# Kernel tuning notes

Hardware: AMD Instinct MI355X
Metric: run time of the kernel (lower is better)

Reference implementation:

```python
import jax, jax.numpy as jnp
import numpy as np

HEADS = 8
DIM_HEAD = 64
NB_FEATURES = 256
CHUNK = 128          # chunk size used by performer's causal_linear_attention_noncuda
EPS_KERNEL = 1e-4    # eps in softmax_kernel feature map
EPS_DENOM = 1e-6     # eps added to k_cumsum in the denominator


def softmax_kernel(data, proj, is_query):
    # FAVOR+ positive softmax random features (performer_pytorch.softmax_kernel)
    # data: [B,H,N,D], proj: [M,D]
    d = data.shape[-1]
    normalizer = d ** -0.25
    ratio = proj.shape[0] ** -0.5
    data_dash = jnp.einsum('bhnd,md->bhnm', data * normalizer, proj)
    # ||x||^2 / (2*sqrt(d))
    diag = jnp.sum(data * data, axis=-1, keepdims=True) * 0.5 * (normalizer ** 2)
    if is_query:
        m = jax.lax.stop_gradient(jnp.max(data_dash, axis=-1, keepdims=True))
    else:
        m = jax.lax.stop_gradient(jnp.max(data_dash, axis=(-1, -2), keepdims=True))
    return ratio * (jnp.exp(data_dash - diag - m) + EPS_KERNEL)


def causal_linear_attention(qp, kp, v, chunk=CHUNK):
    # Chunked causal linear attention (O(N) in seq len):
    # out_i = q'_i . S_i / (q'_i . z_i), S_i = sum_{j<=i} k'_j v_j^T, z_i = cumsum k'_j
    B, H, N, M = qp.shape
    E = v.shape[-1]
    C = N // chunk

    def to_chunks(x):
        return x.reshape(B, H, C, chunk, x.shape[-1]).transpose(2, 0, 1, 3, 4)

    qc, kc, vc = to_chunks(qp), to_chunks(kp), to_chunks(v)
    k0 = jnp.zeros((B, H, M), qp.dtype)
    s0 = jnp.zeros((B, H, M, E), qp.dtype)

    def step(carry, inp):
        k_last, s_last = carry
        q, k, vv = inp  # [B,H,c,M], [B,H,c,M], [B,H,c,E]
        k_cum = k_last[:, :, None, :] + jnp.cumsum(k, axis=2)           # [B,H,c,M]
        d_inv = 1.0 / jnp.einsum('bhnm,bhnm->bhn', q, k_cum + EPS_DENOM)
        ctx = jnp.einsum('bhnm,bhne->bhnme', k, vv)                      # [B,H,c,M,E]
        s_cum = s_last[:, :, None] + jnp.cumsum(ctx, axis=2)             # [B,H,c,M,E]
        out = jnp.einsum('bhnme,bhnm,bhn->bhne', s_cum, q, d_inv)        # [B,H,c,E]
        return (k_cum[:, :, -1, :], s_cum[:, :, -1]), out

    _, outs = jax.lax.scan(step, (k0, s0), (qc, kc, vc))  # [C,B,H,c,E]
    return outs.transpose(1, 2, 0, 3, 4).reshape(B, H, N, E)


def setup_inputs() -> dict:
    key = jax.random.key(0)
    k1, k2, k3, k4 = jax.random.split(key, 4)
    B, N, D = 4, 2048, 512
    return {
        'query': jax.random.normal(k1, (B, N, D), jnp.float32),
        'key': jax.random.normal(k2, (B, N, D), jnp.float32),
        'value': jax.random.normal(k3, (B, N, D), jnp.float32),
        'projection': jax.random.normal(k4, (NB_FEATURES, DIM_HEAD), jnp.float32),
    }


def reference(query, key, value, projection):
    B, N, D = query.shape

    def split(x):  # [B,N,D] -> [B,H,N,Dh]
        return x.reshape(B, N, HEADS, DIM_HEAD).transpose(0, 2, 1, 3)

    q, k, v = split(query), split(key), split(value)
    qp = softmax_kernel(q, projection, is_query=True)
    kp = softmax_kernel(k, projection, is_query=False)
    out = causal_linear_attention(qp, kp, v)
    return out.transpose(0, 2, 1, 3).reshape(B, N, D)
```

## Files before the change

### kernel.cpp

```cpp
#include <hip/hip_runtime.h>
#include <math.h>

#define BB 4
#define NN 2048
#define DD 512
#define HH 8
#define DH 64
#define MM 256
#define BH 32
#define CHK 128
#define NCH 16
#define ROWS (BH*NN)

constexpr float NRM   = 0.35355339059327373f;
constexpr float RATIO = 0.0625f;
constexpr float EPSK  = 1e-4f;
constexpr float EPSD  = 1e-6f;

#define OFFB_QP   ((size_t)0)
#define OFFB_SP   ((size_t)33554432)
#define OFFB_KP   (OFFB_SP + (size_t)16777216)
#define OFFB_VT   (OFFB_KP + (size_t)33554432)
#define OFFB_Z    (OFFB_VT + (size_t)8388608)
#define OFFB_KMP  (OFFB_Z  + (size_t)524288)

typedef __attribute__((ext_vector_type(8))) short short8;
typedef __attribute__((ext_vector_type(4))) float f32x4;

__device__ __forceinline__ float b2f(ushort u) {
  union { float f; unsigned int i; } x; x.i = ((unsigned int)u) << 16; return x.f;
}
__device__ __forceinline__ ushort f2b(float f) {
  unsigned int u = __float_as_uint(f);
  unsigned int r = (u + 0x7FFFu + ((u >> 16) & 1u)) >> 16;
  return (ushort)r;
}

#define MFMA(a,b,c) __builtin_amdgcn_mfma_f32_16x16x32_bf16(a, b, c, 0, 0, 0)

template<int MODE>
__device__ __forceinline__ void featm_body(const float* __restrict__ inp,
                                           const float* __restrict__ proj,
                                           char* __restrict__ ws,
                                           char* lds, int blk) {
  ushort* xh = (ushort*)lds;
  ushort* xl = xh + 64*72;
  ushort* ps = xl + 64*72;
  ushort* qt = ps;
  float* diag_s = (float*)(lds + 55296);
  float (*wmax)[4] = (float(*)[4])(lds + 55552);
  float* kred = (float*)(lds + 56576);

  const int t  = threadIdx.x;
  const int w  = t >> 6;
  const int l  = t & 63;
  const int lq = l >> 4;
  const int ln = l & 15;

  const int rowbase = blk * 64;
  const int bh = rowbase >> 11;
  const int b  = bh >> 3, h = bh & 7;
  const int n0 = rowbase & (NN - 1);

  {
    const int r  = t >> 2;
    const int c0 = (t & 3) * 16;
    const float* src = inp + ((size_t)(b*NN + n0 + r))*DD + h*DH + c0;
    float vv[16];
    #pragma unroll
    for (int j = 0; j < 4; ++j) {
      float4 v = *(const float4*)(src + j*4);
      vv[4*j+0] = v.x*NRM; vv[4*j+1] = v.y*NRM;
      vv[4*j+2] = v.z*NRM; vv[4*j+3] = v.w*NRM;
    }
    float s = 0.f;
    ushort hi[16], lo[16];
    #pragma unroll
    for (int j = 0; j < 16; ++j) {
      s += vv[j]*vv[j];
      hi[j] = f2b(vv[j]);
      lo[j] = f2b(vv[j] - b2f(hi[j]));
    }
    *(short8*)(xh + r*72 + c0)     = *(short8*)&hi[0];
    *(short8*)(xh + r*72 + c0 + 8) = *(short8*)&hi[8];
    *(short8*)(xl + r*72 + c0)     = *(short8*)&lo[0];
    *(short8*)(xl + r*72 + c0 + 8) = *(short8*)&lo[8];
    s += __shfl_xor(s, 1); s += __shfl_xor(s, 2);
    if ((t & 3) == 0) diag_s[r] = 0.5f * s;
  }
  #pragma unroll
  for (int ld = 0; ld < 4; ++ld) {
    int flat = t + 256*ld;
    int r = flat >> 2, c0 = (flat & 3) * 16;
    const float* src = proj + (size_t)r*DH + c0;
    ushort hv[16];
    #pragma unroll
    for (int j = 0; j < 4; ++j) {
      float4 v = *(const float4*)(src + j*4);
      hv[4*j+0] = f2b(v.x); hv[4*j+1] = f2b(v.y);
      hv[4*j+2] = f2b(v.z); hv[4*j+3] = f2b(v.w);
    }
    *(short8*)(ps + r*72 + c0)     = *(short8*)&hv[0];
    *(short8*)(ps + r*72 + c0 + 8) = *(short8*)&hv[8];
  }
  __syncthreads();

  f32x4 acc[4][4];
  #pragma unroll
  for (int mt = 0; mt < 4; ++mt)
    #pragma unroll
    for (int nt = 0; nt < 4; ++nt) acc[mt][nt] = (f32x4){0.f,0.f,0.f,0.f};

  #pragma unroll
  for (int kk = 0; kk < 2; ++kk) {
    short8 ah[4], al[4];
    #pragma unroll
    for (int mt = 0; mt < 4; ++mt) {
      ah[mt] = *(const short8*)(xh + (mt*16 + ln)*72 + kk*32 + lq*8);
      al[mt] = *(const short8*)(xl + (mt*16 + ln)*72 + kk*32 + lq*8);
    }
    #pragma unroll
    for (int nt = 0; nt < 4; ++nt) {
      short8 bf = *(const short8*)(ps + (w*64 + nt*16 + ln)*72 + kk*32 + lq*8);
      #pragma unroll
      for (int mt = 0; mt < 4; ++mt) {
        acc[mt][nt] = MFMA(al[mt], bf, acc[mt][nt]);
        acc[mt][nt] = MFMA(ah[mt], bf, acc[mt][nt]);
      }
    }
  }

  if (MODE == 1) {
    float mx = -1e30f;
    #pragma unroll
    for (int mt = 0; mt < 4; ++mt)
      #pragma unroll
      for (int nt = 0; nt < 4; ++nt)
        #pragma unroll
        for (int reg = 0; reg < 4; ++reg) mx = fmaxf(mx, acc[mt][nt][reg]);
    #pragma unroll
    for (int m = 1; m < 64; m <<= 1) mx = fmaxf(mx, __shfl_xor(mx, m));
    if (l == 0) kred[w] = mx;
    __syncthreads();
    if (t == 0)
      ((float*)(ws + OFFB_KMP))[blk] =
        fmaxf(fmaxf(kred[0], kred[1]), fmaxf(kred[2], kred[3]));
    return;
  }

  if (MODE == 0) {
    #pragma unroll
    for (int mt = 0; mt < 4; ++mt)
      #pragma unroll
      for (int reg = 0; reg < 4; ++reg) {
        float m = acc[mt][0][reg];
        #pragma unroll
        for (int nt = 1; nt < 4; ++nt) m = fmaxf(m, acc[mt][nt][reg]);
        m = fmaxf(m, __shfl_xor(m, 1));
        m = fmaxf(m, __shfl_xor(m, 2));
        m = fmaxf(m, __shfl_xor(m, 4));
        m = fmaxf(m, __shfl_xor(m, 8));
        if (ln == 0) wmax[mt*16 + lq*4 + reg][w] = m;
      }
  }
  if (MODE == 2) {
    if (t < 32) {
      float m = ((const float*)(ws + OFFB_KMP))[bh*32 + t];
      #pragma unroll
      for (int d = 1; d < 32; d <<= 1) m = fmaxf(m, __shfl_xor(m, d));
      if (t == 0) kred[0] = m;
    }
  }
  __syncthreads();

  float km = 0.f;
  if (MODE == 2) km = kred[0];

  #pragma unroll
  for (int mt = 0; mt < 4; ++mt)
    #pragma unroll
    for (int reg = 0; reg < 4; ++reg) {
      const int row = mt*16 + lq*4 + reg;
      float rm;
      if (MODE == 0) {
        float4 wm4 = *(const float4*)&wmax[row][0];
        rm = fmaxf(fmaxf(wm4.x, wm4.y), fmaxf(wm4.z, wm4.w));
      } else {
        rm = km;
      }
      const float dg = diag_s[row];
      #pragma unroll
      for (int nt = 0; nt < 4; ++nt)
        qt[row*264 + w*64 + nt*16 + ln] =
          f2b(RATIO*(expf(acc[mt][nt][reg] - dg - rm) + EPSK));
    }
  __syncthreads();

  ushort* dstbase = (ushort*)(ws + (MODE == 0 ? OFFB_QP : OFFB_KP)) + (size_t)rowbase*MM;
  #pragma unroll
  for (int ld = 0; ld < 8; ++ld) {
    int flat = t + 256*ld;
    int row = flat >> 5, g = flat & 31;
    *(short8*)(dstbase + (size_t)row*MM + g*8) = *(const short8*)(qt + row*264 + g*8);
  }
}

__device__ __forceinline__ void vt_body(const float* __restrict__ value,
                                        char* __restrict__ ws,
                                        char* lds, int blk) {
  float (*vsh)[68] = (float(*)[68])lds;
  const int t = threadIdx.x;
  const int bh = blk >> 4, nc = blk & 15;
  const int b = bh >> 3, h = bh & 7;
  const int n0 = nc * CHK;
  #pragma unroll
  for (int l = 0; l < 8; ++l) {
    int flat = t + 256*l;
    int r = flat >> 4, g = flat & 15;
    *(float4*)&vsh[r][g*4] = *(const float4*)(value + ((size_t)(b*NN + n0 + r))*DD + h*DH + g*4);
  }
  __syncthreads();
  const int e = t & 63, qd = t >> 6;
  ushort* vt = (ushort*)(ws + OFFB_VT) + ((size_t)bh*DH + e)*NN + n0 + qd*32;
  #pragma unroll
  for (int p = 0; p < 16; ++p) {
    unsigned int lo = f2b(vsh[qd*32 + 2*p][e]);
    unsigned int hi = f2b(vsh[qd*32 + 2*p + 1][e]);
    ((unsigned int*)vt)[p] = lo | (hi << 16);
  }
}

__global__ __launch_bounds__(256) void mega_kernel(const float* __restrict__ q,
                                                   const float* __restrict__ k,
                                                   const float* __restrict__ v,
                                                   const float* __restrict__ proj,
                                                   char* __restrict__ ws) {
  __shared__ __align__(16) char lds[56832];
  const int blk = blockIdx.x;
  if (blk < 1024)       featm_body<0>(q, proj, ws, lds, blk);
  else if (blk < 2048)  featm_body<1>(k, proj, ws, lds, blk - 1024);
  else                  vt_body(v, ws, lds, blk - 2048);
}

__global__ __launch_bounds__(256) void featm2_kernel(const float* __restrict__ k,
                                                     const float* __restrict__ proj,
                                                     char* __restrict__ ws) {
  __shared__ __align__(16) char lds[56832];
  featm_body<2>(k, proj, ws, lds, blockIdx.x);
}

__global__ __launch_bounds__(256) void sprefix_kernel(char* __restrict__ ws) {
  __shared__ __align__(16) unsigned int kpTu[32*68];
  __shared__ __align__(16) ushort Vts[64*136];
  __shared__ float zred[8][32];

  const int t  = threadIdx.x;
  const int w  = t >> 6;
  const int l  = t & 63;
  const int lq = l >> 4;
  const int ln = l & 15;
  const int bh = blockIdx.x >> 3;
  const int ms = blockIdx.x & 7;

  const ushort* kpb = (const ushort*)(ws + OFFB_KP) + (size_t)bh*NN*MM + ms*32;
  const ushort* vtb = (const ushort*)(ws + OFFB_VT) + (size_t)bh*DH*NN;
  ushort* spb = (ushort*)(ws + OFFB_SP) + (size_t)bh*NCH*DH*MM + ms*32;
  float*  zb  = (float*)(ws + OFFB_Z) + (size_t)bh*NCH*MM + ms*32;

  f32x4 acc[2];
  acc[0] = (f32x4){0.f,0.f,0.f,0.f};
  acc[1] = (f32x4){0.f,0.f,0.f,0.f};
  float zrun = 0.f;

  for (int tc = 0; tc < NCH; ++tc) {
    __syncthreads();

    if (t < 32) {
      if (tc > 0) {
        float s = 0.f;
        #pragma unroll
        for (int q = 0; q < 8; ++q) s += zred[q][t];
        zrun += s;
      }
      zb[(size_t)tc*MM + t] = zrun;
    }
    {
      ushort* sp = spb + (size_t)tc*DH*MM;
      #pragma unroll
      for (int nt = 0; nt < 2; ++nt)
        #pragma unroll
        for (int reg = 0; reg < 4; ++reg)
          sp[(size_t)(w*16 + lq*4 + reg)*MM + nt*16 + ln] = f2b(acc[nt][reg]);
    }

    const ushort* kslice = kpb + (size_t)tc*CHK*MM;
    {
      int jp = t >> 2, mo = t & 3;
      short8 a = *(const short8*)(kslice + (size_t)(2*jp)*MM + mo*8);
      short8 c = *(const short8*)(kslice + (size_t)(2*jp+1)*MM + mo*8);
      #pragma unroll
      for (int i = 0; i < 8; ++i) {
        unsigned int u = (unsigned int)(unsigned short)a[i]
                       | ((unsigned int)(unsigned short)c[i] << 16);
        kpTu[(mo*8 + i)*68 + jp] = u;
      }
    }
    #pragma unroll
    for (int it = 0; it < 4; ++it) {
      int slot = t + 256*it;
      int e = slot >> 4, g = slot & 15;
      *(short8*)(Vts + e*136 + g*8) = *(const short8*)(vtb + (size_t)e*NN + tc*CHK + g*8);
    }
    __syncthreads();

    {
      int m = t & 31, q = t >> 5;
      float s = 0.f;
      #pragma unroll
      for (int u = 0; u < 8; ++u) {
        unsigned int p = kpTu[m*68 + q*8 + u];
        s += b2f((ushort)(p & 0xFFFF)) + b2f((ushort)(p >> 16));
      }
      zred[q][m] = s;
    }

    #pragma unroll
    for (int kk = 0; kk < 4; ++kk) {
      short8 af = *(const short8*)(Vts + (w*16 + ln)*136 + kk*32 + lq*8);
      #pragma unroll
      for (int nt = 0; nt < 2; ++nt) {
        short8 bf = *(const short8*)((const ushort*)kpTu + (size_t)(nt*16 + ln)*136 + kk*32 + lq*8);
        acc[nt] = MFMA(af, bf, acc[nt]);
      }
    }
  }
}

__global__ __launch_bounds__(256) void fused_kernel(float* __restrict__ out,
                                                    char* __restrict__ ws) {
  __shared__ __align__(16) char lds[52224];
  __shared__ float den_i[128];
  __shared__ float dinv_s[128];

  const int t  = threadIdx.x;
  const int w  = t >> 6;
  const int l  = t & 63;
  const int lq = l >> 4;
  const int ln = l & 15;
  const int rt0 = w;
  const int rt1 = 7 - w;
  const int blk = blockIdx.x;
  const int bh = blk >> 4, tc = blk & 15;
  const int b = bh >> 3, h = bh & 7;
  const size_t rowbase = (size_t)bh*NN + tc*CHK;

  const ushort* qpg = (const ushort*)(ws + OFFB_QP) + rowbase*MM;
  const ushort* kpg = (const ushort*)(ws + OFFB_KP) + rowbase*MM;

  ushort* qs = (ushort*)lds;
  ushort* ks = qs + 128*72;

  f32x4 acc[2][8];
  #pragma unroll
  for (int mt = 0; mt < 2; ++mt)
    #pragma unroll
    for (int nt = 0; nt < 8; ++nt) acc[mt][nt] = (f32x4){0.f,0.f,0.f,0.f};

  for (int mc = 0; mc < 4; ++mc) {
    __syncthreads();
    #pragma unroll
    for (int ld2 = 0; ld2 < 4; ++ld2) {
      int flat = t + 256*ld2; int r = flat >> 3, g = flat & 7;
      *(short8*)(qs + r*72 + g*8) = *(const short8*)(qpg + (size_t)r*MM + mc*64 + g*8);
      *(short8*)(ks + r*72 + g*8) = *(const short8*)(kpg + (size_t)r*MM + mc*64 + g*8);
    }
    __syncthreads();
    #pragma unroll
    for (int kk = 0; kk < 2; ++kk) {
      short8 af0 = *(const short8*)(qs + (rt0*16 + ln)*72 + kk*32 + lq*8);
      short8 af1 = *(const short8*)(qs + (rt1*16 + ln)*72 + kk*32 + lq*8);
      #pragma unroll
      for (int nt = 0; nt < 8; ++nt) {
        if (nt <= rt1) {
          short8 bf = *(const short8*)(ks + (nt*16 + ln)*72 + kk*32 + lq*8);
          if (nt <= rt0) acc[0][nt] = MFMA(af0, bf, acc[0][nt]);
          acc[1][nt] = MFMA(af1, bf, acc[1][nt]);
        }
      }
    }
  }

  __syncthreads();

  ushort* P   = (ushort*)lds;
  ushort* Vts = (ushort*)(lds + 34816);

  float rs[2][4] = {{0,0,0,0},{0,0,0,0}};
  #pragma unroll
  for (int mt = 0; mt < 2; ++mt) {
    const int ibase = (mt ? rt1 : rt0) * 16;
    #pragma unroll
    for (int nt = 0; nt < 8; ++nt)
      #pragma unroll
      for (int reg = 0; reg < 4; ++reg) {
        int i = ibase + lq*4 + reg;
        int j = nt*16 + ln;
        float v = (j <= i) ? acc[mt][nt][reg] : 0.f;
        rs[mt][reg] += v;
        P[i*136 + j] = f2b(v);
      }
  }
  #pragma unroll
  for (int mt = 0; mt < 2; ++mt) {
    const int ibase = (mt ? rt1 : rt0) * 16;
    #pragma unroll
    for (int reg = 0; reg < 4; ++reg) {
      float s = rs[mt][reg];
      s += __shfl_xor(s, 1); s += __shfl_xor(s, 2);
      s += __shfl_xor(s, 4); s += __shfl_xor(s, 8);
      if (ln == 0) den_i[ibase + lq*4 + reg] = s;
    }
  }

  const ushort* vtg = (const ushort*)(ws + OFFB_VT) + (size_t)bh*DH*NN + tc*CHK;
  #pragma unroll
  for (int ld2 = 0; ld2 < 4; ++ld2) {
    int flat = t + 256*ld2; int e = flat >> 4, g = flat & 15;
    *(short8*)(Vts + e*136 + g*8) = *(const short8*)(vtg + (size_t)e*NN + g*8);
  }
  __syncthreads();

  {
    const float* zp = (const float*)(ws + OFFB_Z) + (size_t)blk*MM;
    const int r = t >> 1, hf = t & 1;
    const ushort* qrow = qpg + (size_t)r*MM + hf*128;
    float s = 0.f;
    #pragma unroll
    for (int g = 0; g < 16; ++g) {
      short8 qv = *(const short8*)(qrow + g*8);
      const float* zz = zp + hf*128 + g*8;
      #pragma unroll
      for (int x = 0; x < 8; ++x)
        s += b2f((ushort)qv[x]) * (zz[x] + EPSD);
    }
    s += __shfl_xor(s, 1);
    if (hf == 0) dinv_s[r] = 1.0f / (s + den_i[r]);
  }

  f32x4 oacc[2][4];
  #pragma unroll
  for (int mt = 0; mt < 2; ++mt)
    #pragma unroll
    for (int nt = 0; nt < 4; ++nt) oacc[mt][nt] = (f32x4){0.f,0.f,0.f,0.f};

  #pragma unroll
  for (int kk = 0; kk < 4; ++kk) {
    short8 af0 = *(const short8*)(P + (rt0*16 + ln)*136 + kk*32 + lq*8);
    short8 af1 = *(const short8*)(P + (rt1*16 + ln)*136 + kk*32 + lq*8);
    #pragma unroll
    for (int nt = 0; nt < 4; ++nt) {
      short8 bf = *(const short8*)(Vts + (nt*16 + ln)*136 + kk*32 + lq*8);
      oacc[0][nt] = MFMA(af0, bf, oacc[0][nt]);
      oacc[1][nt] = MFMA(af1, bf, oacc[1][nt]);
    }
  }
  __syncthreads();

  ushort* qs2 = (ushort*)lds;
  ushort* ss  = qs2 + 128*72;
  const ushort* spg = (const ushort*)(ws + OFFB_SP) + (size_t)blk*DH*MM;
  for (int mc = 0; mc < 4; ++mc) {
    if (mc) __syncthreads();
    #pragma unroll
    for (int ld2 = 0; ld2 < 4; ++ld2) {
      int flat = t + 256*ld2; int r = flat >> 3, g = flat & 7;
      *(short8*)(qs2 + r*72 + g*8) = *(const short8*)(qpg + (size_t)r*MM + mc*64 + g*8);
    }
    #pragma unroll
    for (int ld2 = 0; ld2 < 2; ++ld2) {
      int flat = t + 256*ld2; int e = flat >> 3, g = flat & 7;
      *(short8*)(ss + e*72 + g*8) = *(const short8*)(spg + (size_t)e*MM + mc*64 + g*8);
    }
    __syncthreads();
    #pragma unroll
    for (int kk = 0; kk < 2; ++kk) {
      short8 af0 = *(const short8*)(qs2 + (rt0*16 + ln)*72 + kk*32 + lq*8);
      short8 af1 = *(const short8*)(qs2 + (rt1*16 + ln)*72 + kk*32 + lq*8);
      #pragma unroll
      for (int nt = 0; nt < 4; ++nt) {
        short8 bf = *(const short8*)(ss + (nt*16 + ln)*72 + kk*32 + lq*8);
        oacc[0][nt] = MFMA(af0, bf, oacc[0][nt]);
        oacc[1][nt] = MFMA(af1, bf, oacc[1][nt]);
      }
    }
  }

  #pragma unroll
  for (int mt = 0; mt < 2; ++mt) {
    const int ibase = (mt ? rt1 : rt0) * 16;
    #pragma unroll
    for (int reg = 0; reg < 4; ++reg) {
      const int i = ibase + lq*4 + reg;
      const float di = dinv_s[i];
      float* dst = out + ((size_t)(b*NN) + tc*CHK + i)*DD + h*DH;
      #pragma unroll
      for (int nt = 0; nt < 4; ++nt)
        dst[nt*16 + ln] = oacc[mt][nt][reg] * di;
    }
  }
}

extern "C" void kernel_launch(void* const* d_in, const int* in_sizes, int n_in,
                              void* d_out, int out_size, void* d_ws, size_t ws_size,
                              hipStream_t stream) {
  (void)in_sizes; (void)n_in; (void)out_size; (void)ws_size;
  const float* q    = (const float*)d_in[0];
  const float* k    = (const float*)d_in[1];
  const float* v    = (const float*)d_in[2];
  const float* proj = (const float*)d_in[3];
  float* out = (float*)d_out;
  char*  ws  = (char*)d_ws;

  mega_kernel<<<2560, 256, 0, stream>>>(q, k, v, proj, ws);
  featm2_kernel<<<1024, 256, 0, stream>>>(k, proj, ws);
  sprefix_kernel<<<256, 256, 0, stream>>>(ws);
  fused_kernel<<<512, 256, 0, stream>>>(out, ws);
}
```

Baseline: 194.9 us.

## Pre-convert projection to bf16, halve feature-map LDS, and split sprefix finer

A small prep kernel converts the projection matrix to bf16 once, so the feature-map blocks no longer reload and convert it from fp32. The feature-map kernel now stages the projection in two 128-row halves, which cuts its shared memory from about 56KB to 38KB and should allow more resident blocks per CU. It also switches expf to __expf. The sprefix kernel moves from 32 to 16 features per block, doubling the grid to 512 blocks for more parallelism, at the cost of one extra launch and an extra barrier per feature-map block.

Result: faster. 191.0 us (-2.0%).

```diff
diff --git a/kernel.cpp b/kernel.cpp
--- a/kernel.cpp
+++ b/kernel.cpp
@@ -23,6 +23,7 @@
 #define OFFB_VT   (OFFB_KP + (size_t)33554432)
 #define OFFB_Z    (OFFB_VT + (size_t)8388608)
 #define OFFB_KMP  (OFFB_Z  + (size_t)524288)
+#define OFFB_PJB  (OFFB_KMP + (size_t)4096)
 
 typedef __attribute__((ext_vector_type(8))) short short8;
 typedef __attribute__((ext_vector_type(4))) float f32x4;
@@ -38,18 +39,27 @@
 
 #define MFMA(a,b,c) __builtin_amdgcn_mfma_f32_16x16x32_bf16(a, b, c, 0, 0, 0)
 
+__global__ __launch_bounds__(256) void prep_kernel(const float* __restrict__ proj,
+                                                   char* __restrict__ ws) {
+  const int i = blockIdx.x*256 + threadIdx.x;
+  float4 v = *(const float4*)(proj + (size_t)i*4);
+  ushort4 o;
+  o.x = f2b(v.x); o.y = f2b(v.y); o.z = f2b(v.z); o.w = f2b(v.w);
+  *(ushort4*)((ushort*)(ws + OFFB_PJB) + (size_t)i*4) = o;
+}
+
 template<int MODE>
 __device__ __forceinline__ void featm_body(const float* __restrict__ inp,
-                                           const float* __restrict__ proj,
+                                           const ushort* __restrict__ projb,
                                            char* __restrict__ ws,
                                            char* lds, int blk) {
   ushort* xh = (ushort*)lds;
   ushort* xl = xh + 64*72;
   ushort* ps = xl + 64*72;
-  ushort* qt = ps;
-  float* diag_s = (float*)(lds + 55296);
-  float (*wmax)[4] = (float(*)[4])(lds + 55552);
-  float* kred = (float*)(lds + 56576);
+  ushort* qt = (ushort*)lds;
+  float* diag_s = (float*)(lds + 36864);
+  float (*wmax)[4] = (float(*)[4])(lds + 37120);
+  float* kred = (float*)(lds + 38144);
 
   const int t  = threadIdx.x;
   const int w  = t >> 6;
@@ -88,44 +98,39 @@
     s += __shfl_xor(s, 1); s += __shfl_xor(s, 2);
     if ((t & 3) == 0) diag_s[r] = 0.5f * s;
   }
-  #pragma unroll
-  for (int ld = 0; ld < 4; ++ld) {
-    int flat = t + 256*ld;
-    int r = flat >> 2, c0 = (flat & 3) * 16;
-    const float* src = proj + (size_t)r*DH + c0;
-    ushort hv[16];
-    #pragma unroll
-    for (int j = 0; j < 4; ++j) {
-      float4 v = *(const float4*)(src + j*4);
-      hv[4*j+0] = f2b(v.x); hv[4*j+1] = f2b(v.y);
-      hv[4*j+2] = f2b(v.z); hv[4*j+3] = f2b(v.w);
-    }
-    *(short8*)(ps + r*72 + c0)     = *(short8*)&hv[0];
-    *(short8*)(ps + r*72 + c0 + 8) = *(short8*)&hv[8];
-  }
-  __syncthreads();
 
   f32x4 acc[4][4];
   #pragma unroll
   for (int mt = 0; mt < 4; ++mt)
     #pragma unroll
-    for (int nt = 0; nt < 4; ++nt) acc[mt][nt] = (f32x4){0.f,0.f,0.f,0.f};
-
-  #pragma unroll
-  for (int kk = 0; kk < 2; ++kk) {
-    short8 ah[4], al[4];
-    #pragma unroll
-    for (int mt = 0; mt < 4; ++mt) {
-      ah[mt] = *(const short8*)(xh + (mt*16 + ln)*72 + kk*32 + lq*8);
-      al[mt] = *(const short8*)(xl + (mt*16 + ln)*72 + kk*32 + lq*8);
-    }
-    #pragma unroll
-    for (int nt = 0; nt < 4; ++nt) {
-      short8 bf = *(const short8*)(ps + (w*64 + nt*16 + ln)*72 + kk*32 + lq*8);
+    for (int c = 0; c < 4; ++c) acc[mt][c] = (f32x4){0.f,0.f,0.f,0.f};
+
+  #pragma unroll
+  for (int p = 0; p < 2; ++p) {
+    if (p) __syncthreads();
+    #pragma unroll
+    for (int ld = 0; ld < 4; ++ld) {
+      int flat = t + 256*ld;
+      int r = flat >> 3, g = flat & 7;
+      *(short8*)(ps + r*72 + g*8) = *(const short8*)(projb + (size_t)(p*128 + r)*DH + g*8);
+    }
+    __syncthreads();
+    #pragma unroll
+    for (int kk = 0; kk < 2; ++kk) {
+      short8 ah[4], al[4];
       #pragma unroll
       for (int mt = 0; mt < 4; ++mt) {
-        acc[mt][nt] = MFMA(al[mt], bf, acc[mt][nt]);
-        acc[mt][nt] = MFMA(ah[mt], bf, acc[mt][nt]);
+        ah[mt] = *(const short8*)(xh + (mt*16 + ln)*72 + kk*32 + lq*8);
+        al[mt] = *(const short8*)(xl + (mt*16 + ln)*72 + kk*32 + lq*8);
+      }
+      #pragma unroll
+      for (int ntl = 0; ntl < 2; ++ntl) {
+        short8 bf = *(const short8*)(ps + (w*32 + ntl*16 + ln)*72 + kk*32 + lq*8);
+        #pragma unroll
+        for (int mt = 0; mt < 4; ++mt) {
+          acc[mt][2*p+ntl] = MFMA(al[mt], bf, acc[mt][2*p+ntl]);
+          acc[mt][2*p+ntl] = MFMA(ah[mt], bf, acc[mt][2*p+ntl]);
+        }
       }
     }
   }
@@ -135,9 +140,9 @@
     #pragma unroll
     for (int mt = 0; mt < 4; ++mt)
       #pragma unroll
-      for (int nt = 0; nt < 4; ++nt)
+      for (int c = 0; c < 4; ++c)
         #pragma unroll
-        for (int reg = 0; reg < 4; ++reg) mx = fmaxf(mx, acc[mt][nt][reg]);
+        for (int reg = 0; reg < 4; ++reg) mx = fmaxf(mx, acc[mt][c][reg]);
     #pragma unroll
     for (int m = 1; m < 64; m <<= 1) mx = fmaxf(mx, __shfl_xor(mx, m));
     if (l == 0) kred[w] = mx;
@@ -155,7 +160,7 @@
       for (int reg = 0; reg < 4; ++reg) {
         float m = acc[mt][0][reg];
         #pragma unroll
-        for (int nt = 1; nt < 4; ++nt) m = fmaxf(m, acc[mt][nt][reg]);
+        for (int c = 1; c < 4; ++c) m = fmaxf(m, acc[mt][c][reg]);
         m = fmaxf(m, __shfl_xor(m, 1));
         m = fmaxf(m, __shfl_xor(m, 2));
         m = fmaxf(m, __shfl_xor(m, 4));
@@ -190,9 +195,10 @@
       }
       const float dg = diag_s[row];
       #pragma unroll
-      for (int nt = 0; nt < 4; ++nt)
-        qt[row*264 + w*64 + nt*16 + ln] =
-          f2b(RATIO*(expf(acc[mt][nt][reg] - dg - rm) + EPSK));
+      for (int c = 0; c < 4; ++c) {
+        const int f = (c >> 1)*128 + w*32 + (c & 1)*16 + ln;
+        qt[row*264 + f] = f2b(RATIO*(__expf(acc[mt][c][reg] - dg - rm) + EPSK));
+      }
     }
   __syncthreads();
 
@@ -233,53 +239,50 @@
 __global__ __launch_bounds__(256) void mega_kernel(const float* __restrict__ q,
                                                    const float* __restrict__ k,
                                                    const float* __restrict__ v,
-                                                   const float* __restrict__ proj,
                                                    char* __restrict__ ws) {
-  __shared__ __align__(16) char lds[56832];
+  __shared__ __align__(16) char lds[38160];
+  const ushort* projb = (const ushort*)(ws + OFFB_PJB);
   const int blk = blockIdx.x;
-  if (blk < 1024)       featm_body<0>(q, proj, ws, lds, blk);
-  else if (blk < 2048)  featm_body<1>(k, proj, ws, lds, blk - 1024);
+  if (blk < 1024)       featm_body<0>(q, projb, ws, lds, blk);
+  else if (blk < 2048)  featm_body<1>(k, projb, ws, lds, blk - 1024);
   else                  vt_body(v, ws, lds, blk - 2048);
 }
 
 __global__ __launch_bounds__(256) void featm2_kernel(const float* __restrict__ k,
-                                                     const float* __restrict__ proj,
                                                      char* __restrict__ ws) {
-  __shared__ __align__(16) char lds[56832];
-  featm_body<2>(k, proj, ws, lds, blockIdx.x);
+  __shared__ __align__(16) char lds[38160];
+  featm_body<2>(k, (const ushort*)(ws + OFFB_PJB), ws, lds, blockIdx.x);
 }
 
 __global__ __launch_bounds__(256) void sprefix_kernel(char* __restrict__ ws) {
-  __shared__ __align__(16) unsigned int kpTu[32*68];
+  __shared__ __align__(16) unsigned int kpTu[16*68];
   __shared__ __align__(16) ushort Vts[64*136];
-  __shared__ float zred[8][32];
+  __shared__ float zred[16][16];
 
   const int t  = threadIdx.x;
   const int w  = t >> 6;
   const int l  = t & 63;
   const int lq = l >> 4;
   const int ln = l & 15;
-  const int bh = blockIdx.x >> 3;
-  const int ms = blockIdx.x & 7;
-
-  const ushort* kpb = (const ushort*)(ws + OFFB_KP) + (size_t)bh*NN*MM + ms*32;
+  const int bh = blockIdx.x >> 4;
+  const int ms = blockIdx.x & 15;
+
+  const ushort* kpb = (const ushort*)(ws + OFFB_KP) + (size_t)bh*NN*MM + ms*16;
   const ushort* vtb = (const ushort*)(ws + OFFB_VT) + (size_t)bh*DH*NN;
-  ushort* spb = (ushort*)(ws + OFFB_SP) + (size_t)bh*NCH*DH*MM + ms*32;
-  float*  zb  = (float*)(ws + OFFB_Z) + (size_t)bh*NCH*MM + ms*32;
-
-  f32x4 acc[2];
-  acc[0] = (f32x4){0.f,0.f,0.f,0.f};
-  acc[1] = (f32x4){0.f,0.f,0.f,0.f};
+  ushort* spb = (ushort*)(ws + OFFB_SP) + (size_t)bh*NCH*DH*MM + ms*16;
+  float*  zb  = (float*)(ws + OFFB_Z) + (size_t)bh*NCH*MM + ms*16;
+
+  f32x4 acc = (f32x4){0.f,0.f,0.f,0.f};
   float zrun = 0.f;
 
   for (int tc = 0; tc < NCH; ++tc) {
     __syncthreads();
 
-    if (t < 32) {
+    if (t < 16) {
       if (tc > 0) {
         float s = 0.f;
         #pragma unroll
-        for (int q = 0; q < 8; ++q) s += zred[q][t];
+        for (int q = 0; q < 16; ++q) s += zred[q][t];
         zrun += s;
       }
       zb[(size_t)tc*MM + t] = zrun;
@@ -287,15 +290,13 @@
     {
       ushort* sp = spb + (size_t)tc*DH*MM;
       #pragma unroll
-      for (int nt = 0; nt < 2; ++nt)
-        #pragma unroll
-        for (int reg = 0; reg < 4; ++reg)
-          sp[(size_t)(w*16 + lq*4 + reg)*MM + nt*16 + ln] = f2b(acc[nt][reg]);
+      for (int reg = 0; reg < 4; ++reg)
+        sp[(size_t)(w*16 + lq*4 + reg)*MM + ln] = f2b(acc[reg]);
     }
 
     const ushort* kslice = kpb + (size_t)tc*CHK*MM;
-    {
-      int jp = t >> 2, mo = t & 3;
+    if (t < 128) {
+      int jp = t >> 1, mo = t & 1;
       short8 a = *(const short8*)(kslice + (size_t)(2*jp)*MM + mo*8);
       short8 c = *(const short8*)(kslice + (size_t)(2*jp+1)*MM + mo*8);
       #pragma unroll
@@ -314,11 +315,11 @@
     __syncthreads();
 
     {
-      int m = t & 31, q = t >> 5;
+      int m = t & 15, q = t >> 4;
       float s = 0.f;
       #pragma unroll
-      for (int u = 0; u < 8; ++u) {
-        unsigned int p = kpTu[m*68 + q*8 + u];
+      for (int u = 0; u < 4; ++u) {
+        unsigned int p = kpTu[m*68 + q*4 + u];
         s += b2f((ushort)(p & 0xFFFF)) + b2f((ushort)(p >> 16));
       }
       zred[q][m] = s;
@@ -327,11 +328,8 @@
     #pragma unroll
     for (int kk = 0; kk < 4; ++kk) {
       short8 af = *(const short8*)(Vts + (w*16 + ln)*136 + kk*32 + lq*8);
-      #pragma unroll
-      for (int nt = 0; nt < 2; ++nt) {
-        short8 bf = *(const short8*)((const ushort*)kpTu + (size_t)(nt*16 + ln)*136 + kk*32 + lq*8);
-        acc[nt] = MFMA(af, bf, acc[nt]);
-      }
+      short8 bf = *(const short8*)((const ushort*)kpTu + (size_t)ln*136 + kk*32 + lq*8);
+      acc = MFMA(af, bf, acc);
     }
   }
 }
@@ -521,8 +519,9 @@
   float* out = (float*)d_out;
   char*  ws  = (char*)d_ws;
 
-  mega_kernel<<<2560, 256, 0, stream>>>(q, k, v, proj, ws);
-  featm2_kernel<<<1024, 256, 0, stream>>>(k, proj, ws);
-  sprefix_kernel<<<256, 256, 0, stream>>>(ws);
+  prep_kernel<<<16, 256, 0, stream>>>(proj, ws);
+  mega_kernel<<<2560, 256, 0, stream>>>(q, k, v, ws);
+  featm2_kernel<<<1024, 256, 0, stream>>>(k, ws);
+  sprefix_kernel<<<512, 256, 0, stream>>>(ws);
   fused_kernel<<<512, 256, 0, stream>>>(out, ws);
 }
```
